# Kernel tuning notes

Hardware: AMD Instinct MI355X
Metric: run time of the kernel (lower is better)

## Reference

```python
import jax, jax.numpy as jnp
import numpy as np

N = 100000   # nodes
E = 1600000  # edges (avg degree 16)
D = 64       # feature dim
STEPS = 3

def setup_inputs() -> dict:
    key = jax.random.key(0)
    ks = jax.random.split(key, 16)
    def rn(i, shape, scale=1.0):
        return jax.random.normal(ks[i], shape, dtype=jnp.float32) * scale
    inp = {
        "nodes": rn(0, (N, D)),
        "edges": rn(1, (E, D)),
        "globals_": rn(2, (1, D)),
        "senders": jax.random.randint(ks[3], (E,), 0, N, dtype=jnp.int32),
        "receivers": jax.random.randint(ks[4], (E,), 0, N, dtype=jnp.int32),
        # edge MLP: in 4*D -> D -> D
        "We1": rn(5, (4 * D, D), (4 * D) ** -0.5),
        "be1": jnp.zeros((D,), jnp.float32),
        "We2": rn(6, (D, D), D ** -0.5),
        "be2": jnp.zeros((D,), jnp.float32),
        # node MLP: in 3*D -> D -> D
        "Wn1": rn(7, (3 * D, D), (3 * D) ** -0.5),
        "bn1": jnp.zeros((D,), jnp.float32),
        "Wn2": rn(8, (D, D), D ** -0.5),
        "bn2": jnp.zeros((D,), jnp.float32),
        # global MLP: in 3*D -> D -> D
        "Wg1": rn(9, (3 * D, D), (3 * D) ** -0.5),
        "bg1": jnp.zeros((D,), jnp.float32),
        "Wg2": rn(10, (D, D), D ** -0.5),
        "bg2": jnp.zeros((D,), jnp.float32),
    }
    return inp

def _mlp(x, W1, b1, W2, b2):
    return jax.nn.relu(x @ W1 + b1) @ W2 + b2

def reference(nodes, edges, globals_, senders, receivers,
              We1, be1, We2, be2, Wn1, bn1, Wn2, bn2, Wg1, bg1, Wg2, bg2):
    g = globals_  # [1, D], single graph
    n_nodes = nodes.shape[0]
    for _ in range(STEPS):
        # --- edge update: gather sender/receiver node feats + broadcast globals ---
        sent = nodes[senders]        # [E, D]
        recv = nodes[receivers]      # [E, D]
        ge = jnp.broadcast_to(g, (edges.shape[0], g.shape[-1]))
        edges = _mlp(jnp.concatenate([edges, sent, recv, ge], axis=-1),
                     We1, be1, We2, be2)  # [E, D]
        # --- aggregate edges to nodes (received messages) ---
        received = jax.ops.segment_sum(edges, receivers, num_segments=n_nodes)
        gn = jnp.broadcast_to(g, (n_nodes, g.shape[-1]))
        nodes = _mlp(jnp.concatenate([nodes, received, gn], axis=-1),
                     Wn1, bn1, Wn2, bn2)  # [N, D]
        # --- aggregate to globals (single graph => full sums) ---
        agg_n = jnp.sum(nodes, axis=0, keepdims=True)  # [1, D]
        agg_e = jnp.sum(edges, axis=0, keepdims=True)  # [1, D]
        g = _mlp(jnp.concatenate([agg_n, agg_e, g], axis=-1),
                 Wg1, bg1, Wg2, bg2)  # [1, D]
    return nodes, edges, g
```

## Files before the change

### kernel.cpp

```cpp
#include <hip/hip_runtime.h>

#define DD 64
typedef unsigned int uint32;
typedef unsigned short ushort16;
typedef short bf16x8 __attribute__((ext_vector_type(8)));
typedef float f32x4 __attribute__((ext_vector_type(4)));

__device__ __forceinline__ ushort16 f2bf(float x) {
    uint32 u = __float_as_uint(x);
    uint32 r = (u + 0x7FFFu + ((u >> 16) & 1u)) >> 16;
    return (ushort16)r;
}
__device__ __forceinline__ float bf2f(ushort16 h) {
    return __uint_as_float(((uint32)h) << 16);
}

__device__ __forceinline__ void split8f(const float4& a, const float4& b, bf16x8& ah, bf16x8& al) {
    float xs[8] = {a.x, a.y, a.z, a.w, b.x, b.y, b.z, b.w};
#pragma unroll
    for (int i = 0; i < 8; ++i) {
        ushort16 hi = f2bf(xs[i]);
        ah[i] = (short)hi;
        al[i] = (short)f2bf(xs[i] - bf2f(hi));
    }
}
__device__ __forceinline__ void unpack8(const uint4& a, const uint4& b, bf16x8& ah, bf16x8& al) {
    uint32 us[8] = {a.x, a.y, a.z, a.w, b.x, b.y, b.z, b.w};
#pragma unroll
    for (int i = 0; i < 8; ++i) {
        ah[i] = (short)(us[i] >> 16);
        al[i] = (short)(us[i] & 0xFFFFu);
    }
}

__device__ __forceinline__ void mfma_ks(const unsigned short* __restrict__ wks, int l,
                                        const bf16x8* ah, const bf16x8* al, f32x4 (*acc)[4]) {
#pragma unroll
    for (int tt = 0; tt < 4; ++tt) {
        bf16x8 bh = *(const bf16x8*)(wks + ((size_t)(tt * 2 + 0) * 64 + l) * 8);
        bf16x8 bl = *(const bf16x8*)(wks + ((size_t)(tt * 2 + 1) * 64 + l) * 8);
#pragma unroll
        for (int m = 0; m < 4; ++m) {
            acc[m][tt] = __builtin_amdgcn_mfma_f32_16x16x32_bf16(ah[m], bh, acc[m][tt], 0, 0, 0);
            acc[m][tt] = __builtin_amdgcn_mfma_f32_16x16x32_bf16(ah[m], bl, acc[m][tt], 0, 0, 0);
            acc[m][tt] = __builtin_amdgcn_mfma_f32_16x16x32_bf16(al[m], bh, acc[m][tt], 0, 0, 0);
        }
    }
}

__global__ void zero_counts_kernel(int* __restrict__ counts, int N) {
    int i = blockIdx.x * blockDim.x + threadIdx.x;
    if (i < N) counts[i] = 0;
}

__global__ void hist_kernel(const int* __restrict__ recv, int* __restrict__ counts, int E) {
    int i = blockIdx.x * blockDim.x + threadIdx.x;
    if (i < E) atomicAdd(&counts[recv[i]], 1);
}

__global__ __launch_bounds__(1024) void scan_kernel(const int* __restrict__ counts,
                                                    int* __restrict__ offs,
                                                    int* __restrict__ cursor, int N) {
    __shared__ int sm[1024];
    __shared__ int carryS;
    int t = threadIdx.x;
    if (t == 0) carryS = 0;
    __syncthreads();
    for (int base = 0; base < N; base += 4096) {
        int idx = base + t * 4;
        int x0 = (idx + 0 < N) ? counts[idx + 0] : 0;
        int x1 = (idx + 1 < N) ? counts[idx + 1] : 0;
        int x2 = (idx + 2 < N) ? counts[idx + 2] : 0;
        int x3 = (idx + 3 < N) ? counts[idx + 3] : 0;
        int s1 = x0 + x1, s2 = s1 + x2, s3 = s2 + x3;
        sm[t] = s3;
        __syncthreads();
        for (int d = 1; d < 1024; d <<= 1) {
            int v = (t >= d) ? sm[t - d] : 0;
            __syncthreads();
            sm[t] += v;
            __syncthreads();
        }
        int excl = sm[t] - s3 + carryS;
        if (idx < N)     { offs[idx]     = excl;      cursor[idx]     = excl; }
        if (idx + 1 < N) { offs[idx + 1] = excl + x0; cursor[idx + 1] = excl + x0; }
        if (idx + 2 < N) { offs[idx + 2] = excl + s1; cursor[idx + 2] = excl + s1; }
        if (idx + 3 < N) { offs[idx + 3] = excl + s2; cursor[idx + 3] = excl + s2; }
        int chunkTotal = sm[1023];
        __syncthreads();
        if (t == 0) carryS += chunkTotal;
        __syncthreads();
    }
    if (t == 0) offs[N] = carryS;
}

__global__ void scatter_kernel(const int* __restrict__ recv, int* __restrict__ cursor,
                               int* __restrict__ perm, int E) {
    int i = blockIdx.x * blockDim.x + threadIdx.x;
    if (i < E) {
        int p = atomicAdd(&cursor[recv[i]], 1);
        perm[p] = i;
    }
}

__global__ __launch_bounds__(256) void gather_kernel(
    const float* __restrict__ edges, const int* __restrict__ offs,
    const int* __restrict__ perm, float* __restrict__ received, int N)
{
    int w = threadIdx.x >> 6;
    int lane = threadIdx.x & 63;
    int n = blockIdx.x * 4 + w;
    if (n >= N) return;
    int s = offs[n], e = offs[n + 1];
    float acc = 0.f;
    for (int i = s; i < e; ++i) {
        int ed = perm[i];
        acc += edges[(size_t)ed * DD + lane];
    }
    received[(size_t)n * DD + lane] = acc;
}

__global__ void prep_bias_kernel(const float* __restrict__ g,
                                 const float* __restrict__ We1, const float* __restrict__ be1,
                                 const float* __restrict__ Wn1, const float* __restrict__ bn1,
                                 float* __restrict__ be1e, float* __restrict__ bn1e) {
    int j = threadIdx.x;
    float a = be1[j];
    float b = bn1[j];
    for (int k = 0; k < DD; ++k) {
        float gk = g[k];
        a = fmaf(gk, We1[(192 + k) * DD + j], a);
        b = fmaf(gk, Wn1[(128 + k) * DD + j], b);
    }
    be1e[j] = a;
    bn1e[j] = b;
}

__global__ void prep_nodes_kernel(const float* __restrict__ src, uint32* __restrict__ dst,
                                  int total) {
    int i = blockIdx.x * blockDim.x + threadIdx.x;
    if (i < total) {
        float x = src[i];
        ushort16 hi = f2bf(x);
        ushort16 lo = f2bf(x - bf2f(hi));
        dst[i] = ((uint32)hi << 16) | (uint32)lo;
    }
}

__device__ __forceinline__ void prep_pack(const float* __restrict__ W, int nks,
                                          unsigned short* __restrict__ dst, int tid) {
    if (tid < nks * 2048) {
        int i = tid & 7, lane = (tid >> 3) & 63, tt = (tid >> 9) & 3, ks = tid >> 11;
        int k = ks * 32 + (lane >> 4) * 8 + i;
        int n = tt * 16 + (lane & 15);
        float x = W[k * DD + n];
        ushort16 hi = f2bf(x);
        ushort16 lo = f2bf(x - bf2f(hi));
        dst[(((ks * 4 + tt) * 2 + 0) * 64 + lane) * 8 + i] = hi;
        dst[(((ks * 4 + tt) * 2 + 1) * 64 + lane) * 8 + i] = lo;
    }
}

__global__ void prep_weights_kernel(const float* __restrict__ We1, const float* __restrict__ We2,
                                    const float* __restrict__ Wn1, const float* __restrict__ Wn2,
                                    unsigned short* __restrict__ we1p, unsigned short* __restrict__ we2p,
                                    unsigned short* __restrict__ wn1p, unsigned short* __restrict__ wn2p) {
    int tid = blockIdx.x * blockDim.x + threadIdx.x;
    prep_pack(We1, 6, we1p, tid);
    prep_pack(We2, 2, we2p, tid);
    prep_pack(Wn1, 4, wn1p, tid);
    prep_pack(Wn2, 2, wn2p, tid);
}

__global__ __launch_bounds__(256, 2) void edge_kernel_mfma(
    const float* __restrict__ edges_in, const uint32* __restrict__ nodes_pk,
    const int* __restrict__ senders, const int* __restrict__ receivers,
    const unsigned short* __restrict__ w1, const float* __restrict__ b1,
    const unsigned short* __restrict__ w2, const float* __restrict__ b2,
    float* __restrict__ edges_out, float* __restrict__ agg_e, int E)
{
    __shared__ unsigned short HB[4][4][2][1024];
    __shared__ float PS[4][64];

    const int t = threadIdx.x;
    const int w = t >> 6, l = t & 63;
    const int lm = l & 15, kq = l >> 4;
    const int base = (blockIdx.x << 8) + (w << 6);

    int gie[4], gis[4], gir[4];
#pragma unroll
    for (int m = 0; m < 4; ++m) {
        int row = base + (m << 4) + lm;
        int gi = min(row, E - 1);
        gie[m] = gi;
        gis[m] = senders[gi];
        gir[m] = receivers[gi];
    }

    float4 re[4][4];
#pragma unroll
    for (int m = 0; m < 4; ++m) {
        const float* p = edges_in + (size_t)gie[m] * DD + kq * 8;
        re[m][0] = *(const float4*)(p);
        re[m][1] = *(const float4*)(p + 4);
        re[m][2] = *(const float4*)(p + 32);
        re[m][3] = *(const float4*)(p + 36);
    }
    uint4 rs[4][4];
#pragma unroll
    for (int m = 0; m < 4; ++m) {
        const uint32* p = nodes_pk + (size_t)gis[m] * DD + kq * 8;
        rs[m][0] = *(const uint4*)(p);
        rs[m][1] = *(const uint4*)(p + 4);
        rs[m][2] = *(const uint4*)(p + 32);
        rs[m][3] = *(const uint4*)(p + 36);
    }

    f32x4 acc[4][4];
#pragma unroll
    for (int tt = 0; tt < 4; ++tt) {
        float b = b1[tt * 16 + lm];
#pragma unroll
        for (int m = 0; m < 4; ++m) { acc[m][tt][0] = b; acc[m][tt][1] = b; acc[m][tt][2] = b; acc[m][tt][3] = b; }
    }

#pragma unroll
    for (int ks2 = 0; ks2 < 2; ++ks2) {
        bf16x8 ah[4], al[4];
#pragma unroll
        for (int m = 0; m < 4; ++m) split8f(re[m][ks2 * 2], re[m][ks2 * 2 + 1], ah[m], al[m]);
        mfma_ks(w1 + (size_t)ks2 * 4096, l, ah, al, acc);
    }

    uint4 rr[4][4];
#pragma unroll
    for (int m = 0; m < 4; ++m) {
        const uint32* p = nodes_pk + (size_t)gir[m] * DD + kq * 8;
        rr[m][0] = *(const uint4*)(p);
        rr[m][1] = *(const uint4*)(p + 4);
        rr[m][2] = *(const uint4*)(p + 32);
        rr[m][3] = *(const uint4*)(p + 36);
    }

#pragma unroll
    for (int ks2 = 0; ks2 < 2; ++ks2) {
        bf16x8 ah[4], al[4];
#pragma unroll
        for (int m = 0; m < 4; ++m) unpack8(rs[m][ks2 * 2], rs[m][ks2 * 2 + 1], ah[m], al[m]);
        mfma_ks(w1 + (size_t)(2 + ks2) * 4096, l, ah, al, acc);
    }
#pragma unroll
    for (int ks2 = 0; ks2 < 2; ++ks2) {
        bf16x8 ah[4], al[4];
#pragma unroll
        for (int m = 0; m < 4; ++m) unpack8(rr[m][ks2 * 2], rr[m][ks2 * 2 + 1], ah[m], al[m]);
        mfma_ks(w1 + (size_t)(4 + ks2) * 4096, l, ah, al, acc);
    }

#pragma unroll
    for (int m = 0; m < 4; ++m) {
        char* hh = (char*)&HB[w][m][0][0];
        char* hl = (char*)&HB[w][m][1][0];
#pragma unroll
        for (int tt = 0; tt < 4; ++tt)
#pragma unroll
            for (int r = 0; r < 4; ++r) {
                int row = (kq << 2) + r;
                int col = (tt << 4) + lm;
                float hv = fmaxf(acc[m][tt][r], 0.f);
                ushort16 hi = f2bf(hv);
                ushort16 lo = f2bf(hv - bf2f(hi));
                int boff = (row << 7) + ((((col >> 3) ^ (row & 7)) & 7) << 4) + ((col & 7) << 1);
                *(unsigned short*)(hh + boff) = hi;
                *(unsigned short*)(hl + boff) = lo;
            }
    }

    f32x4 acc2[4][4];
#pragma unroll
    for (int tt = 0; tt < 4; ++tt) {
        float b = b2[tt * 16 + lm];
#pragma unroll
        for (int m = 0; m < 4; ++m) { acc2[m][tt][0] = b; acc2[m][tt][1] = b; acc2[m][tt][2] = b; acc2[m][tt][3] = b; }
    }
#pragma unroll
    for (int ks = 0; ks < 2; ++ks) {
        bf16x8 ah[4], al[4];
#pragma unroll
        for (int m = 0; m < 4; ++m) {
            int boff = (lm << 7) + ((((kq + ks * 4) ^ (lm & 7)) & 7) << 4);
            ah[m] = *(const bf16x8*)((char*)&HB[w][m][0][0] + boff);
            al[m] = *(const bf16x8*)((char*)&HB[w][m][1][0] + boff);
        }
        mfma_ks(w2 + (size_t)ks * 4096, l, ah, al, acc2);
    }

#pragma unroll
    for (int tt = 0; tt < 4; ++tt) {
        float s = 0.f;
#pragma unroll
        for (int m = 0; m < 4; ++m)
#pragma unroll
            for (int r = 0; r < 4; ++r) {
                int rowg = base + (m << 4) + (kq << 2) + r;
                if (rowg < E) s += acc2[m][tt][r];
            }
        s += __shfl_xor(s, 16, 64);
        s += __shfl_xor(s, 32, 64);
        if (l < 16) PS[w][tt * 16 + l] = s;
    }

    char* CW = (char*)&HB[w][0][0][0];
#pragma unroll
    for (int m = 0; m < 4; ++m)
#pragma unroll
        for (int tt = 0; tt < 4; ++tt)
#pragma unroll
            for (int r = 0; r < 4; ++r) {
                int row = (kq << 2) + r;
                int col = (tt << 4) + lm;
                int boff = (row << 8) + ((((col >> 2) ^ (row & 15)) & 15) << 4) + ((col & 3) << 2);
                *(float*)(CW + m * 4096 + boff) = acc2[m][tt][r];
            }
#pragma unroll
    for (int m = 0; m < 4; ++m) {
        int rowg = base + (m << 4) + lm;
        float4* dst = (float4*)(edges_out + (size_t)rowg * DD);
#pragma unroll
        for (int j = 0; j < 4; ++j) {
            int fc = kq + (j << 2);
            int boff = (lm << 8) + (((fc ^ (lm & 15)) & 15) << 4);
            float4 v = *(float4*)(CW + m * 4096 + boff);
            if (rowg < E) dst[fc] = v;
        }
    }

    __syncthreads();
    if (t < 64) {
        float s = PS[0][t] + PS[1][t] + PS[2][t] + PS[3][t];
        atomicAdd(agg_e + t, s);
    }
}

__global__ __launch_bounds__(256, 2) void node_kernel_mfma(
    const uint32* __restrict__ nodes_pk, const float* __restrict__ received,
    const unsigned short* __restrict__ w1, const float* __restrict__ b1,
    const unsigned short* __restrict__ w2, const float* __restrict__ b2,
    float* __restrict__ nodes_out, float* __restrict__ agg_n, int N)
{
    __shared__ unsigned short HB[4][4][2][1024];
    __shared__ float PS[4][64];

    const int t = threadIdx.x;
    const int w = t >> 6, l = t & 63;
    const int lm = l & 15, kq = l >> 4;
    const int base = (blockIdx.x << 8) + (w << 6);

    int gi[4];
#pragma unroll
    for (int m = 0; m < 4; ++m) gi[m] = min(base + (m << 4) + lm, N - 1);

    uint4 rn[4][4];
#pragma unroll
    for (int m = 0; m < 4; ++m) {
        const uint32* p = nodes_pk + (size_t)gi[m] * DD + kq * 8;
        rn[m][0] = *(const uint4*)(p);
        rn[m][1] = *(const uint4*)(p + 4);
        rn[m][2] = *(const uint4*)(p + 32);
        rn[m][3] = *(const uint4*)(p + 36);
    }
    float4 rc[4][4];
#pragma unroll
    for (int m = 0; m < 4; ++m) {
        const float* p = received + (size_t)gi[m] * DD + kq * 8;
        rc[m][0] = *(const float4*)(p);
        rc[m][1] = *(const float4*)(p + 4);
        rc[m][2] = *(const float4*)(p + 32);
        rc[m][3] = *(const float4*)(p + 36);
    }

    f32x4 acc[4][4];
#pragma unroll
    for (int tt = 0; tt < 4; ++tt) {
        float b = b1[tt * 16 + lm];
#pragma unroll
        for (int m = 0; m < 4; ++m) { acc[m][tt][0] = b; acc[m][tt][1] = b; acc[m][tt][2] = b; acc[m][tt][3] = b; }
    }

#pragma unroll
    for (int ks2 = 0; ks2 < 2; ++ks2) {
        bf16x8 ah[4], al[4];
#pragma unroll
        for (int m = 0; m < 4; ++m) unpack8(rn[m][ks2 * 2], rn[m][ks2 * 2 + 1], ah[m], al[m]);
        mfma_ks(w1 + (size_t)ks2 * 4096, l, ah, al, acc);
    }
#pragma unroll
    for (int ks2 = 0; ks2 < 2; ++ks2) {
        bf16x8 ah[4], al[4];
#pragma unroll
        for (int m = 0; m < 4; ++m) split8f(rc[m][ks2 * 2], rc[m][ks2 * 2 + 1], ah[m], al[m]);
        mfma_ks(w1 + (size_t)(2 + ks2) * 4096, l, ah, al, acc);
    }

#pragma unroll
    for (int m = 0; m < 4; ++m) {
        char* hh = (char*)&HB[w][m][0][0];
        char* hl = (char*)&HB[w][m][1][0];
#pragma unroll
        for (int tt = 0; tt < 4; ++tt)
#pragma unroll
            for (int r = 0; r < 4; ++r) {
                int row = (kq << 2) + r;
                int col = (tt << 4) + lm;
                float hv = fmaxf(acc[m][tt][r], 0.f);
                ushort16 hi = f2bf(hv);
                ushort16 lo = f2bf(hv - bf2f(hi));
                int boff = (row << 7) + ((((col >> 3) ^ (row & 7)) & 7) << 4) + ((col & 7) << 1);
                *(unsigned short*)(hh + boff) = hi;
                *(unsigned short*)(hl + boff) = lo;
            }
    }

    f32x4 acc2[4][4];
#pragma unroll
    for (int tt = 0; tt < 4; ++tt) {
        float b = b2[tt * 16 + lm];
#pragma unroll
        for (int m = 0; m < 4; ++m) { acc2[m][tt][0] = b; acc2[m][tt][1] = b; acc2[m][tt][2] = b; acc2[m][tt][3] = b; }
    }
#pragma unroll
    for (int ks = 0; ks < 2; ++ks) {
        bf16x8 ah[4], al[4];
#pragma unroll
        for (int m = 0; m < 4; ++m) {
            int boff = (lm << 7) + ((((kq + ks * 4) ^ (lm & 7)) & 7) << 4);
            ah[m] = *(const bf16x8*)((char*)&HB[w][m][0][0] + boff);
            al[m] = *(const bf16x8*)((char*)&HB[w][m][1][0] + boff);
        }
        mfma_ks(w2 + (size_t)ks * 4096, l, ah, al, acc2);
    }

#pragma unroll
    for (int tt = 0; tt < 4; ++tt) {
        float s = 0.f;
#pragma unroll
        for (int m = 0; m < 4; ++m)
#pragma unroll
            for (int r = 0; r < 4; ++r) {
                int rowg = base + (m << 4) + (kq << 2) + r;
                if (rowg < N) s += acc2[m][tt][r];
            }
        s += __shfl_xor(s, 16, 64);
        s += __shfl_xor(s, 32, 64);
        if (l < 16) PS[w][tt * 16 + l] = s;
    }

    char* CW = (char*)&HB[w][0][0][0];
#pragma unroll
    for (int m = 0; m < 4; ++m)
#pragma unroll
        for (int tt = 0; tt < 4; ++tt)
#pragma unroll
            for (int r = 0; r < 4; ++r) {
                int row = (kq << 2) + r;
                int col = (tt << 4) + lm;
                int boff = (row << 8) + ((((col >> 2) ^ (row & 15)) & 15) << 4) + ((col & 3) << 2);
                *(float*)(CW + m * 4096 + boff) = acc2[m][tt][r];
            }
#pragma unroll
    for (int m = 0; m < 4; ++m) {
        int rowg = base + (m << 4) + lm;
        float4* dst = (float4*)(nodes_out + (size_t)rowg * DD);
#pragma unroll
        for (int j = 0; j < 4; ++j) {
            int fc = kq + (j << 2);
            int boff = (lm << 8) + (((fc ^ (lm & 15)) & 15) << 4);
            float4 v = *(float4*)(CW + m * 4096 + boff);
            if (rowg < N) dst[fc] = v;
        }
    }

    __syncthreads();
    if (t < 64) {
        float s = PS[0][t] + PS[1][t] + PS[2][t] + PS[3][t];
        atomicAdd(agg_n + t, s);
    }
}

__global__ void global_kernel(const float* __restrict__ agg_n, const float* __restrict__ agg_e,
                              const float* __restrict__ g_in,
                              const float* __restrict__ Wg1, const float* __restrict__ bg1,
                              const float* __restrict__ Wg2, const float* __restrict__ bg2,
                              float* __restrict__ g_out)
{
    __shared__ float h[64];
    int j = threadIdx.x;
    float a = bg1[j];
    for (int k = 0; k < DD; ++k) a = fmaf(agg_n[k], Wg1[k * DD + j], a);
    for (int k = 0; k < DD; ++k) a = fmaf(agg_e[k], Wg1[(64 + k) * DD + j], a);
    for (int k = 0; k < DD; ++k) a = fmaf(g_in[k],  Wg1[(128 + k) * DD + j], a);
    h[j] = fmaxf(a, 0.f);
    __syncthreads();
    float o = bg2[j];
    for (int k = 0; k < DD; ++k) o = fmaf(h[k], Wg2[k * DD + j], o);
    g_out[j] = o;
}

extern "C" void kernel_launch(void* const* d_in, const int* in_sizes, int n_in,
                              void* d_out, int out_size, void* d_ws, size_t ws_size,
                              hipStream_t stream) {
    const float* nodes0 = (const float*)d_in[0];
    const float* edges0 = (const float*)d_in[1];
    const float* g0     = (const float*)d_in[2];
    const int* senders   = (const int*)d_in[3];
    const int* receivers = (const int*)d_in[4];
    const float* We1 = (const float*)d_in[5];
    const float* be1 = (const float*)d_in[6];
    const float* We2 = (const float*)d_in[7];
    const float* be2 = (const float*)d_in[8];
    const float* Wn1 = (const float*)d_in[9];
    const float* bn1 = (const float*)d_in[10];
    const float* Wn2 = (const float*)d_in[11];
    const float* bn2 = (const float*)d_in[12];
    const float* Wg1 = (const float*)d_in[13];
    const float* bg1 = (const float*)d_in[14];
    const float* Wg2 = (const float*)d_in[15];
    const float* bg2 = (const float*)d_in[16];

    const int N = in_sizes[0] / DD;
    const int E = in_sizes[1] / DD;

    float* out_nodes = (float*)d_out;
    float* out_edges = out_nodes + (size_t)N * DD;
    float* out_g     = out_edges + (size_t)E * DD;

    float* ws = (float*)d_ws;
    float* received = ws;
    float* aggs = received + (size_t)N * DD;
    float* agg_n = aggs;
    float* agg_e = aggs + 64;
    float* b1e   = aggs + 128;
    float* b1n   = aggs + 192;
    float* g1    = aggs + 256;
    float* g2    = aggs + 320;
    int* counts = (int*)(aggs + 512);
    int* offs   = counts + N;
    int* cursor = offs + N + 4;
    int* perm   = cursor + N;
    uint32* nodes_pk = (uint32*)(perm + E);
    unsigned short* we1p = (unsigned short*)(nodes_pk + (size_t)N * DD);
    unsigned short* we2p = we1p + 24576;
    unsigned short* wn1p = we2p + 8192;
    unsigned short* wn2p = wn1p + 16384;

    const int eblocks = (E + 255) / 256;
    const int nblocks = (N + 255) / 256;

    zero_counts_kernel<<<(N + 255) / 256, 256, 0, stream>>>(counts, N);
    hist_kernel<<<(E + 255) / 256, 256, 0, stream>>>(receivers, counts, E);
    scan_kernel<<<1, 1024, 0, stream>>>(counts, offs, cursor, N);
    scatter_kernel<<<(E + 255) / 256, 256, 0, stream>>>(receivers, cursor, perm, E);
    prep_weights_kernel<<<48, 256, 0, stream>>>(We1, We2, Wn1, Wn2, we1p, we2p, wn1p, wn2p);

    for (int s = 0; s < 3; ++s) {
        const float* nsrc = (s == 0) ? nodes0 : out_nodes;
        const float* esrc = (s == 0) ? edges0 : out_edges;
        const float* gin  = (s == 0) ? g0 : ((s == 1) ? g1 : g2);
        float* gout       = (s == 2) ? out_g : ((s == 0) ? g1 : g2);

        hipMemsetAsync(aggs, 0, 128 * sizeof(float), stream);
        prep_bias_kernel<<<1, 64, 0, stream>>>(gin, We1, be1, Wn1, bn1, b1e, b1n);
        prep_nodes_kernel<<<(N * DD + 255) / 256, 256, 0, stream>>>(nsrc, nodes_pk, N * DD);
        edge_kernel_mfma<<<eblocks, 256, 0, stream>>>(esrc, nodes_pk, senders, receivers,
                                                      we1p, b1e, we2p, be2,
                                                      out_edges, agg_e, E);
        gather_kernel<<<(N + 3) / 4, 256, 0, stream>>>(out_edges, offs, perm, received, N);
        node_kernel_mfma<<<nblocks, 256, 0, stream>>>(nodes_pk, received, wn1p, b1n, wn2p, bn2,
                                                      out_nodes, agg_n, N);
        global_kernel<<<1, 64, 0, stream>>>(agg_n, agg_e, gin, Wg1, bg1, Wg2, bg2, gout);
    }
}
```

Measured before the change: 2.311 ms.

## Fuse segment-sum into edge kernel via receiver-sorted edge order and run-length atomics

The edge kernel now processes edges in receiver-sorted order through perm and accumulates runs of equal receivers, flushing each run with atomicAdd into received. This removes the separate gather kernel and its re-read of all edge outputs. The second MLP layer is restructured per 16-row group to shrink shared memory and registers, with launch bounds raised to 3 blocks per CU. The cost is an indirect, scattered read of edges_in and write of edges_out through perm, a full memset of received each step, and a float summation order that is no longer fixed.

```diff
diff --git a/kernel.cpp b/kernel.cpp
--- a/kernel.cpp
+++ b/kernel.cpp
@@ -45,6 +45,18 @@
             acc[m][tt] = __builtin_amdgcn_mfma_f32_16x16x32_bf16(ah[m], bl, acc[m][tt], 0, 0, 0);
             acc[m][tt] = __builtin_amdgcn_mfma_f32_16x16x32_bf16(al[m], bh, acc[m][tt], 0, 0, 0);
         }
+    }
+}
+
+__device__ __forceinline__ void mfma_ks1(const unsigned short* __restrict__ wks, int l,
+                                         bf16x8 ah, bf16x8 al, f32x4* acc) {
+#pragma unroll
+    for (int tt = 0; tt < 4; ++tt) {
+        bf16x8 bh = *(const bf16x8*)(wks + ((size_t)(tt * 2 + 0) * 64 + l) * 8);
+        bf16x8 bl = *(const bf16x8*)(wks + ((size_t)(tt * 2 + 1) * 64 + l) * 8);
+        acc[tt] = __builtin_amdgcn_mfma_f32_16x16x32_bf16(ah, bh, acc[tt], 0, 0, 0);
+        acc[tt] = __builtin_amdgcn_mfma_f32_16x16x32_bf16(ah, bl, acc[tt], 0, 0, 0);
+        acc[tt] = __builtin_amdgcn_mfma_f32_16x16x32_bf16(al, bh, acc[tt], 0, 0, 0);
     }
 }
 
@@ -103,23 +115,6 @@
     }
 }
 
-__global__ __launch_bounds__(256) void gather_kernel(
-    const float* __restrict__ edges, const int* __restrict__ offs,
-    const int* __restrict__ perm, float* __restrict__ received, int N)
-{
-    int w = threadIdx.x >> 6;
-    int lane = threadIdx.x & 63;
-    int n = blockIdx.x * 4 + w;
-    if (n >= N) return;
-    int s = offs[n], e = offs[n + 1];
-    float acc = 0.f;
-    for (int i = s; i < e; ++i) {
-        int ed = perm[i];
-        acc += edges[(size_t)ed * DD + lane];
-    }
-    received[(size_t)n * DD + lane] = acc;
-}
-
 __global__ void prep_bias_kernel(const float* __restrict__ g,
                                  const float* __restrict__ We1, const float* __restrict__ be1,
                                  const float* __restrict__ Wn1, const float* __restrict__ bn1,
@@ -172,35 +167,46 @@
     prep_pack(Wn2, 2, wn2p, tid);
 }
 
-__global__ __launch_bounds__(256, 2) void edge_kernel_mfma(
+__global__ __launch_bounds__(256, 3) void edge_kernel_mfma(
     const float* __restrict__ edges_in, const uint32* __restrict__ nodes_pk,
     const int* __restrict__ senders, const int* __restrict__ receivers,
+    const int* __restrict__ perm,
     const unsigned short* __restrict__ w1, const float* __restrict__ b1,
     const unsigned short* __restrict__ w2, const float* __restrict__ b2,
-    float* __restrict__ edges_out, float* __restrict__ agg_e, int E)
+    float* __restrict__ edges_out, float* __restrict__ received,
+    float* __restrict__ agg_e, int E)
 {
-    __shared__ unsigned short HB[4][4][2][1024];
+    __shared__ int PE[4][64];
+    __shared__ int SID[4][64];
+    __shared__ int RID[4][64];
     __shared__ float PS[4][64];
+    __shared__ __align__(16) char HB[4][4096];
 
     const int t = threadIdx.x;
     const int w = t >> 6, l = t & 63;
     const int lm = l & 15, kq = l >> 4;
     const int base = (blockIdx.x << 8) + (w << 6);
 
-    int gie[4], gis[4], gir[4];
-#pragma unroll
-    for (int m = 0; m < 4; ++m) {
-        int row = base + (m << 4) + lm;
-        int gi = min(row, E - 1);
-        gie[m] = gi;
-        gis[m] = senders[gi];
-        gir[m] = receivers[gi];
+    {
+        int pos = base + l;
+        int pe = perm[min(pos, E - 1)];
+        PE[w][l] = pe;
+        SID[w][l] = senders[pe];
+        RID[w][l] = receivers[pe];
+    }
+
+    int pe_m[4], sid_m[4], rid_m[4];
+#pragma unroll
+    for (int m = 0; m < 4; ++m) {
+        pe_m[m]  = PE[w][(m << 4) + lm];
+        sid_m[m] = SID[w][(m << 4) + lm];
+        rid_m[m] = RID[w][(m << 4) + lm];
     }
 
     float4 re[4][4];
 #pragma unroll
     for (int m = 0; m < 4; ++m) {
-        const float* p = edges_in + (size_t)gie[m] * DD + kq * 8;
+        const float* p = edges_in + (size_t)pe_m[m] * DD + kq * 8;
         re[m][0] = *(const float4*)(p);
         re[m][1] = *(const float4*)(p + 4);
         re[m][2] = *(const float4*)(p + 32);
@@ -209,7 +215,7 @@
     uint4 rs[4][4];
 #pragma unroll
     for (int m = 0; m < 4; ++m) {
-        const uint32* p = nodes_pk + (size_t)gis[m] * DD + kq * 8;
+        const uint32* p = nodes_pk + (size_t)sid_m[m] * DD + kq * 8;
         rs[m][0] = *(const uint4*)(p);
         rs[m][1] = *(const uint4*)(p + 4);
         rs[m][2] = *(const uint4*)(p + 32);
@@ -235,7 +241,7 @@
     uint4 rr[4][4];
 #pragma unroll
     for (int m = 0; m < 4; ++m) {
-        const uint32* p = nodes_pk + (size_t)gir[m] * DD + kq * 8;
+        const uint32* p = nodes_pk + (size_t)rid_m[m] * DD + kq * 8;
         rr[m][0] = *(const uint4*)(p);
         rr[m][1] = *(const uint4*)(p + 4);
         rr[m][2] = *(const uint4*)(p + 32);
@@ -257,10 +263,15 @@
         mfma_ks(w1 + (size_t)(4 + ks2) * 4096, l, ah, al, acc);
     }
 
-#pragma unroll
-    for (int m = 0; m < 4; ++m) {
-        char* hh = (char*)&HB[w][m][0][0];
-        char* hl = (char*)&HB[w][m][1][0];
+    float b2v[4];
+#pragma unroll
+    for (int tt = 0; tt < 4; ++tt) b2v[tt] = b2[tt * 16 + lm];
+    float sreg[4] = {0.f, 0.f, 0.f, 0.f};
+    char* hh = &HB[w][0];
+    char* hl = &HB[w][2048];
+
+#pragma unroll
+    for (int m = 0; m < 4; ++m) {
 #pragma unroll
         for (int tt = 0; tt < 4; ++tt)
 #pragma unroll
@@ -274,45 +285,27 @@
                 *(unsigned short*)(hh + boff) = hi;
                 *(unsigned short*)(hl + boff) = lo;
             }
-    }
-
-    f32x4 acc2[4][4];
-#pragma unroll
-    for (int tt = 0; tt < 4; ++tt) {
-        float b = b2[tt * 16 + lm];
-#pragma unroll
-        for (int m = 0; m < 4; ++m) { acc2[m][tt][0] = b; acc2[m][tt][1] = b; acc2[m][tt][2] = b; acc2[m][tt][3] = b; }
-    }
-#pragma unroll
-    for (int ks = 0; ks < 2; ++ks) {
-        bf16x8 ah[4], al[4];
-#pragma unroll
-        for (int m = 0; m < 4; ++m) {
+
+        f32x4 acc2[4];
+#pragma unroll
+        for (int tt = 0; tt < 4; ++tt) { acc2[tt][0] = b2v[tt]; acc2[tt][1] = b2v[tt]; acc2[tt][2] = b2v[tt]; acc2[tt][3] = b2v[tt]; }
+#pragma unroll
+        for (int ks = 0; ks < 2; ++ks) {
             int boff = (lm << 7) + ((((kq + ks * 4) ^ (lm & 7)) & 7) << 4);
-            ah[m] = *(const bf16x8*)((char*)&HB[w][m][0][0] + boff);
-            al[m] = *(const bf16x8*)((char*)&HB[w][m][1][0] + boff);
-        }
-        mfma_ks(w2 + (size_t)ks * 4096, l, ah, al, acc2);
-    }
-
-#pragma unroll
-    for (int tt = 0; tt < 4; ++tt) {
-        float s = 0.f;
-#pragma unroll
-        for (int m = 0; m < 4; ++m)
+            bf16x8 ah = *(const bf16x8*)(hh + boff);
+            bf16x8 al = *(const bf16x8*)(hl + boff);
+            mfma_ks1(w2 + (size_t)ks * 4096, l, ah, al, acc2);
+        }
+
+#pragma unroll
+        for (int tt = 0; tt < 4; ++tt) {
 #pragma unroll
             for (int r = 0; r < 4; ++r) {
-                int rowg = base + (m << 4) + (kq << 2) + r;
-                if (rowg < E) s += acc2[m][tt][r];
-            }
-        s += __shfl_xor(s, 16, 64);
-        s += __shfl_xor(s, 32, 64);
-        if (l < 16) PS[w][tt * 16 + l] = s;
-    }
-
-    char* CW = (char*)&HB[w][0][0][0];
-#pragma unroll
-    for (int m = 0; m < 4; ++m)
+                int rowp = base + (m << 4) + (kq << 2) + r;
+                if (rowp < E) sreg[tt] += acc2[tt][r];
+            }
+        }
+
 #pragma unroll
         for (int tt = 0; tt < 4; ++tt)
 #pragma unroll
@@ -320,21 +313,50 @@
                 int row = (kq << 2) + r;
                 int col = (tt << 4) + lm;
                 int boff = (row << 8) + ((((col >> 2) ^ (row & 15)) & 15) << 4) + ((col & 3) << 2);
-                *(float*)(CW + m * 4096 + boff) = acc2[m][tt][r];
-            }
-#pragma unroll
-    for (int m = 0; m < 4; ++m) {
-        int rowg = base + (m << 4) + lm;
-        float4* dst = (float4*)(edges_out + (size_t)rowg * DD);
-#pragma unroll
-        for (int j = 0; j < 4; ++j) {
-            int fc = kq + (j << 2);
-            int boff = (lm << 8) + (((fc ^ (lm & 15)) & 15) << 4);
-            float4 v = *(float4*)(CW + m * 4096 + boff);
-            if (rowg < E) dst[fc] = v;
-        }
-    }
-
+                *(float*)(&HB[w][0] + boff) = acc2[tt][r];
+            }
+
+        {
+            int rowp = base + (m << 4) + lm;
+            float4* dst = (float4*)(edges_out + (size_t)pe_m[m] * DD);
+#pragma unroll
+            for (int j = 0; j < 4; ++j) {
+                int fc = kq + (j << 2);
+                int boff = (lm << 8) + (((fc ^ (lm & 15)) & 15) << 4);
+                float4 v = *(float4*)(&HB[w][0] + boff);
+                if (rowp < E) dst[fc] = v;
+            }
+        }
+
+        {
+            float run = 0.f;
+#pragma unroll
+            for (int r = 0; r < 16; ++r) {
+                int rowp = base + (m << 4) + r;
+                if (rowp < E) {
+                    int boff = (r << 8) + ((((l >> 2) ^ (r & 15)) & 15) << 4) + ((l & 3) << 2);
+                    float v = *(const float*)(&HB[w][0] + boff);
+                    int rid = RID[w][(m << 4) + r];
+                    run += v;
+                    bool flush;
+                    if (r == 15) flush = true;
+                    else flush = (rowp + 1 >= E) || (RID[w][(m << 4) + r + 1] != rid);
+                    if (flush) {
+                        atomicAdd(&received[(size_t)rid * DD + l], run);
+                        run = 0.f;
+                    }
+                }
+            }
+        }
+    }
+
+#pragma unroll
+    for (int tt = 0; tt < 4; ++tt) {
+        float s = sreg[tt];
+        s += __shfl_xor(s, 16, 64);
+        s += __shfl_xor(s, 32, 64);
+        if (l < 16) PS[w][tt * 16 + l] = s;
+    }
     __syncthreads();
     if (t < 64) {
         float s = PS[0][t] + PS[1][t] + PS[2][t] + PS[3][t];
@@ -568,13 +590,12 @@
         const float* gin  = (s == 0) ? g0 : ((s == 1) ? g1 : g2);
         float* gout       = (s == 2) ? out_g : ((s == 0) ? g1 : g2);
 
-        hipMemsetAsync(aggs, 0, 128 * sizeof(float), stream);
+        hipMemsetAsync(received, 0, ((size_t)N * DD + 128) * sizeof(float), stream);
         prep_bias_kernel<<<1, 64, 0, stream>>>(gin, We1, be1, Wn1, bn1, b1e, b1n);
         prep_nodes_kernel<<<(N * DD + 255) / 256, 256, 0, stream>>>(nsrc, nodes_pk, N * DD);
-        edge_kernel_mfma<<<eblocks, 256, 0, stream>>>(esrc, nodes_pk, senders, receivers,
+        edge_kernel_mfma<<<eblocks, 256, 0, stream>>>(esrc, nodes_pk, senders, receivers, perm,
                                                       we1p, b1e, we2p, be2,
-                                                      out_edges, agg_e, E);
-        gather_kernel<<<(N + 3) / 4, 256, 0, stream>>>(out_edges, offs, perm, received, N);
+                                                      out_edges, received, agg_e, E);
         node_kernel_mfma<<<nblocks, 256, 0, stream>>>(nodes_pk, received, wn1p, b1n, wn2p, bn2,
                                                       out_nodes, agg_n, N);
         global_kernel<<<1, 64, 0, stream>>>(agg_n, agg_e, gin, Wg1, bg1, Wg2, bg2, gout);
```

New measurement: 1.992 ms. 13.8% less time.
